# Optimization experiments

Measured on AMD Instinct MI355X. Metric: run time of the kernel, lower is better.

## Reference

```python
import jax, jax.numpy as jnp
import numpy as np

STRIDE = 16


def setup_inputs() -> dict:
    key = jax.random.key(0)
    kq, kk, kv, km = jax.random.split(key, 4)
    B, H, T, D = 2, 16, 2048, 64
    q = jax.random.normal(kq, (B, H, T, D), dtype=jnp.float32)
    k = jax.random.normal(kk, (B, H, T, D), dtype=jnp.float32)
    v = jax.random.normal(kv, (B, H, T, D), dtype=jnp.float32)
    mask = jax.random.randint(km, (B, 1, 1, T), 0, 2, dtype=jnp.int32)
    return {"q": q, "k": k, "v": v, "mask": mask}


def reference(q, k, v, mask):
    # q,k,v: (B,H,T,D); mask: (B,1,1,T_k)
    B, H, T_q, D = q.shape
    T_k = k.shape[2]
    scale = 1.0 / jnp.sqrt(jnp.float32(D))
    scores = jnp.einsum("bhqd,bhkd->bhqk", q, k) * scale
    rq = jnp.arange(T_q)[:, None]
    rk = jnp.arange(T_k)[None, :]
    stride_mask = (rk % STRIDE == 0) | (rq == rk)           # (T_q, T_k) bool
    NEG = jnp.float32(-1e9)
    scores = jnp.where(stride_mask[None, None], scores, NEG)
    scores = jnp.where(mask == 0, NEG, scores)
    attn = jax.nn.softmax(scores, axis=-1)
    out = jnp.einsum("bhqk,bhkd->bhqd", attn, v)
    return (out, attn)
```

## Files before the change

kernel.cpp:

```cpp
#include <hip/hip_runtime.h>
#include <hip/hip_bf16.h>

constexpr int B = 2, H = 16, T = 2048, D = 64;
constexpr int NS = T / 16;
constexpr int WAVES = 4, BLOCK = 256;
constexpr int CHUNKS = 32;
constexpr int ROWS_PER_BLOCK = T / CHUNKS;
constexpr int ROWS_PER_WAVE = ROWS_PER_BLOCK / WAVES;
constexpr int R = 4;
constexpr int GROUPS = ROWS_PER_WAVE / R;

__device__ __forceinline__ float rlf(float v, int l) {
    return __int_as_float(__builtin_amdgcn_readlane(__float_as_int(v), l));
}
__device__ __forceinline__ unsigned bf16rne(float f) {
    unsigned x = __float_as_uint(f);
    return (x + 0x7fffu + ((x >> 16) & 1u)) >> 16;
}
__device__ __forceinline__ float bflo(unsigned u) { return __uint_as_float(u << 16); }
__device__ __forceinline__ float bfhi(unsigned u) { return __uint_as_float(u & 0xffff0000u); }

__global__ __launch_bounds__(BLOCK, 4)
void strided_attn_kernel(const float* __restrict__ q,
                         const float* __restrict__ k,
                         const float* __restrict__ v,
                         const int*   __restrict__ mask,
                         float* __restrict__ out,
                         float* __restrict__ attn)
{
    __shared__ uint2    Ks2[NS][16];
    __shared__ unsigned Vp[NS / 2][64];
    __shared__ int      msk[NS];

    const int blk   = blockIdx.x;
    const int bh    = blk / CHUNKS;
    const int chunk = blk % CHUNKS;
    const int b     = bh / H;

    const float* qb = q + (size_t)bh * T * D;
    const float* kb = k + (size_t)bh * T * D;
    const float* vb = v + (size_t)bh * T * D;
    const int*   mb = mask + (size_t)b * T;

    const int tid = threadIdx.x;

    for (int i = tid; i < NS * 16; i += BLOCK) {
        const int j = i >> 4, c = i & 15;
        const float4 kv = *reinterpret_cast<const float4*>(kb + (size_t)(j * 16) * D + c * 4);
        uint2 pk;
        pk.x = bf16rne(kv.x) | (bf16rne(kv.y) << 16);
        pk.y = bf16rne(kv.z) | (bf16rne(kv.w) << 16);
        Ks2[j][c ^ (j & 15)] = pk;
    }
    for (int i = tid; i < (NS / 2) * 64; i += BLOCK) {
        const int j2 = i >> 6, d = i & 63;
        const float f0 = vb[(size_t)(32 * j2) * D + d];
        const float f1 = vb[(size_t)(32 * j2 + 16) * D + d];
        Vp[j2][d] = bf16rne(f0) | (bf16rne(f1) << 16);
    }
    if (tid < NS) msk[tid] = mb[tid * 16];

    const int wave = tid >> 6, lane = tid & 63;
    const int row0 = chunk * ROWS_PER_BLOCK + wave * ROWS_PER_WAVE;
    const int j0 = lane, j1 = lane + 64;
    const int xsw = lane & 15;
    const size_t bhT = (size_t)bh * T;

    const int mvals = (lane < ROWS_PER_WAVE) ? mb[row0 + lane] : 0;

    __syncthreads();

    const int m0 = msk[j0], m1 = msk[j1];

    #pragma unroll 1
    for (int g = 0; g < GROUPS; ++g) {
        const int grow = row0 + g * R;

        const float4 qv = *reinterpret_cast<const float4*>(qb + (size_t)grow * D + lane * 4);
        const float4 kg = *reinterpret_cast<const float4*>(kb + (size_t)grow * D + lane * 4);
        float vdr[R];
        #pragma unroll
        for (int r = 0; r < R; ++r)
            vdr[r] = vb[(size_t)(grow + r) * D + lane];

        float ds = fmaf(qv.w, kg.w, fmaf(qv.z, kg.z, fmaf(qv.y, kg.y, qv.x * kg.x)));
        ds += __shfl_xor(ds, 1, 64);
        ds += __shfl_xor(ds, 2, 64);
        ds += __shfl_xor(ds, 4, 64);
        ds += __shfl_xor(ds, 8, 64);
        const float sdv = ds * 0.125f;

        float s0[R] = {0.f, 0.f, 0.f, 0.f};
        float s1[R] = {0.f, 0.f, 0.f, 0.f};
        #pragma unroll 4
        for (int cq = 0; cq < 16; ++cq) {
            const uint2 a0 = Ks2[j0][cq ^ xsw];
            const uint2 a1 = Ks2[j1][cq ^ xsw];
            const float k0x = bflo(a0.x), k0y = bfhi(a0.x), k0z = bflo(a0.y), k0w = bfhi(a0.y);
            const float k1x = bflo(a1.x), k1y = bfhi(a1.x), k1z = bflo(a1.y), k1w = bfhi(a1.y);
            #pragma unroll
            for (int r = 0; r < R; ++r) {
                const int src = 16 * r + cq;
                const float qx = rlf(qv.x, src);
                const float qy = rlf(qv.y, src);
                const float qz = rlf(qv.z, src);
                const float qw = rlf(qv.w, src);
                s0[r] = fmaf(qw, k0w, fmaf(qz, k0z, fmaf(qy, k0y, fmaf(qx, k0x, s0[r]))));
                s1[r] = fmaf(qw, k1w, fmaf(qz, k1z, fmaf(qy, k1y, fmaf(qx, k1x, s1[r]))));
            }
        }

        float p0[R], p1[R], pd[R];
        #pragma unroll
        for (int r = 0; r < R; ++r) {
            float a0 = s0[r] * 0.125f, a1 = s1[r] * 0.125f;
            if (m0 == 0) a0 = -1e9f;
            if (m1 == 0) a1 = -1e9f;

            float sd = rlf(sdv, 16 * r);
            if (__builtin_amdgcn_readlane(mvals, g * R + r) == 0) sd = -1e9f;
            const bool qmod = (((g * R + r) & 15) == 0);

            const float e0 = __expf(a0);
            const float e1 = __expf(a1);
            const float ed = qmod ? 0.f : __expf(sd);
            float sum = e0 + e1;
            #pragma unroll
            for (int s = 32; s > 0; s >>= 1) sum += __shfl_xor(sum, s, 64);
            sum += ed;
            const float inv = 1.f / sum;

            p0[r] = e0 * inv;
            p1[r] = e1 * inv;
            pd[r] = ed * inv;
        }

        float acc[R];
        #pragma unroll
        for (int r = 0; r < R; ++r)
            acc[r] = pd[r] * vdr[r];

        #pragma unroll 8
        for (int j2 = 0; j2 < 32; ++j2) {
            const unsigned u = Vp[j2][lane];
            const float ve = bflo(u), vo = bfhi(u);
            #pragma unroll
            for (int r = 0; r < R; ++r)
                acc[r] = fmaf(rlf(p0[r], 2 * j2 + 1), vo,
                         fmaf(rlf(p0[r], 2 * j2), ve, acc[r]));
        }
        #pragma unroll 8
        for (int j2 = 32; j2 < 64; ++j2) {
            const unsigned u = Vp[j2][lane];
            const float ve = bflo(u), vo = bfhi(u);
            #pragma unroll
            for (int r = 0; r < R; ++r)
                acc[r] = fmaf(rlf(p1[r], 2 * (j2 - 32) + 1), vo,
                         fmaf(rlf(p1[r], 2 * (j2 - 32)), ve, acc[r]));
        }

        #pragma unroll
        for (int r = 0; r < R; ++r)
            out[(bhT + grow + r) * D + lane] = acc[r];

        #pragma unroll 1
        for (int t = 0; t < 8; ++t) {
            const int f    = t * 64 + lane;
            const int idx2 = ((t & 3) * 16) + (lane >> 2);
            #pragma unroll
            for (int r = 0; r < R; ++r) {
                const int qrow = grow + r;
                const float psrc = (t < 4) ? p0[r] : p1[r];
                const float pg   = __shfl(psrc, idx2, 64);
                float4 val = make_float4(0.f, 0.f, 0.f, 0.f);
                if ((lane & 3) == 0) val.x = pg;
                const bool qmod = (((g * R + r) & 15) == 0);
                const int  fq   = qrow >> 2;
                if (!qmod && t == (fq >> 6) && lane == (fq & 63)) {
                    if      (r == 0) val.x = pd[r];
                    else if (r == 1) val.y = pd[r];
                    else if (r == 2) val.z = pd[r];
                    else             val.w = pd[r];
                }
                *reinterpret_cast<float4*>(attn + (bhT + qrow) * (size_t)T + 4 * f) = val;
            }
        }
    }
}

extern "C" void kernel_launch(void* const* d_in, const int* in_sizes, int n_in,
                              void* d_out, int out_size, void* d_ws, size_t ws_size,
                              hipStream_t stream) {
    const float* q    = (const float*)d_in[0];
    const float* k    = (const float*)d_in[1];
    const float* v    = (const float*)d_in[2];
    const int*   mask = (const int*)d_in[3];

    float* out  = (float*)d_out;
    float* attn = out + (size_t)B * H * T * D;

    dim3 grid(B * H * CHUNKS);
    dim3 block(BLOCK);
    hipLaunchKernelGGL(strided_attn_kernel, grid, block, 0, stream,
                       q, k, v, mask, out, attn);
}
```

Baseline: 145.3 us.

## Process eight query rows per group, preload Q, and reswizzle K LDS layout

Doubles the rows handled per group from four to eight, so each K read from LDS and each V read are reused across twice as many query rows. All four Q row-vectors the wave needs are loaded once before the loop instead of reloading Q per group. The K shared-memory swizzle gains an extra XOR term meant to cut bank conflicts. The cost is more registers for the accumulators and probabilities, which may hurt occupancy under the launch-bounds limit.

```diff
diff --git a/kernel.cpp b/kernel.cpp
--- a/kernel.cpp
+++ b/kernel.cpp
@@ -7,7 +7,7 @@
 constexpr int CHUNKS = 32;
 constexpr int ROWS_PER_BLOCK = T / CHUNKS;
 constexpr int ROWS_PER_WAVE = ROWS_PER_BLOCK / WAVES;
-constexpr int R = 4;
+constexpr int R = 8;
 constexpr int GROUPS = ROWS_PER_WAVE / R;
 
 __device__ __forceinline__ float rlf(float v, int l) {
@@ -19,6 +19,10 @@
 }
 __device__ __forceinline__ float bflo(unsigned u) { return __uint_as_float(u << 16); }
 __device__ __forceinline__ float bfhi(unsigned u) { return __uint_as_float(u & 0xffff0000u); }
+
+__device__ __forceinline__ int kslot(int c, int j) {
+    return c ^ (j & 15) ^ (((j >> 4) & 3) << 2);
+}
 
 __global__ __launch_bounds__(BLOCK, 4)
 void strided_attn_kernel(const float* __restrict__ q,
@@ -50,7 +54,7 @@
         uint2 pk;
         pk.x = bf16rne(kv.x) | (bf16rne(kv.y) << 16);
         pk.y = bf16rne(kv.z) | (bf16rne(kv.w) << 16);
-        Ks2[j][c ^ (j & 15)] = pk;
+        Ks2[j][kslot(c, j)] = pk;
     }
     for (int i = tid; i < (NS / 2) * 64; i += BLOCK) {
         const int j2 = i >> 6, d = i & 63;
@@ -63,10 +67,15 @@
     const int wave = tid >> 6, lane = tid & 63;
     const int row0 = chunk * ROWS_PER_BLOCK + wave * ROWS_PER_WAVE;
     const int j0 = lane, j1 = lane + 64;
-    const int xsw = lane & 15;
+    const int xsw = (lane & 15) ^ (((lane >> 4) & 3) << 2);
     const size_t bhT = (size_t)bh * T;
 
     const int mvals = (lane < ROWS_PER_WAVE) ? mb[row0 + lane] : 0;
+
+    const float4 qv0  = *reinterpret_cast<const float4*>(qb + (size_t)(row0     ) * D + lane * 4);
+    const float4 qv20 = *reinterpret_cast<const float4*>(qb + (size_t)(row0 +  4) * D + lane * 4);
+    const float4 qv1  = *reinterpret_cast<const float4*>(qb + (size_t)(row0 +  8) * D + lane * 4);
+    const float4 qv21 = *reinterpret_cast<const float4*>(qb + (size_t)(row0 + 12) * D + lane * 4);
 
     __syncthreads();
 
@@ -76,22 +85,19 @@
     for (int g = 0; g < GROUPS; ++g) {
         const int grow = row0 + g * R;
 
-        const float4 qv = *reinterpret_cast<const float4*>(qb + (size_t)grow * D + lane * 4);
-        const float4 kg = *reinterpret_cast<const float4*>(kb + (size_t)grow * D + lane * 4);
+        const float4 kg  = *reinterpret_cast<const float4*>(kb + (size_t)(grow    ) * D + lane * 4);
+        const float4 kg2 = *reinterpret_cast<const float4*>(kb + (size_t)(grow + 4) * D + lane * 4);
         float vdr[R];
         #pragma unroll
         for (int r = 0; r < R; ++r)
             vdr[r] = vb[(size_t)(grow + r) * D + lane];
 
-        float ds = fmaf(qv.w, kg.w, fmaf(qv.z, kg.z, fmaf(qv.y, kg.y, qv.x * kg.x)));
-        ds += __shfl_xor(ds, 1, 64);
-        ds += __shfl_xor(ds, 2, 64);
-        ds += __shfl_xor(ds, 4, 64);
-        ds += __shfl_xor(ds, 8, 64);
-        const float sdv = ds * 0.125f;
-
-        float s0[R] = {0.f, 0.f, 0.f, 0.f};
-        float s1[R] = {0.f, 0.f, 0.f, 0.f};
+        const float4 qsel  = (g == 0) ? qv0  : qv1;
+        const float4 qsel2 = (g == 0) ? qv20 : qv21;
+
+        float s0[R], s1[R];
+        #pragma unroll
+        for (int r = 0; r < R; ++r) { s0[r] = 0.f; s1[r] = 0.f; }
         #pragma unroll 4
         for (int cq = 0; cq < 16; ++cq) {
             const uint2 a0 = Ks2[j0][cq ^ xsw];
@@ -100,15 +106,28 @@
             const float k1x = bflo(a1.x), k1y = bfhi(a1.x), k1z = bflo(a1.y), k1w = bfhi(a1.y);
             #pragma unroll
             for (int r = 0; r < R; ++r) {
-                const int src = 16 * r + cq;
-                const float qx = rlf(qv.x, src);
-                const float qy = rlf(qv.y, src);
-                const float qz = rlf(qv.z, src);
-                const float qw = rlf(qv.w, src);
+                const int src = 16 * (r & 3) + cq;
+                const float qx = rlf((r < 4) ? qsel.x : qsel2.x, src);
+                const float qy = rlf((r < 4) ? qsel.y : qsel2.y, src);
+                const float qz = rlf((r < 4) ? qsel.z : qsel2.z, src);
+                const float qw = rlf((r < 4) ? qsel.w : qsel2.w, src);
                 s0[r] = fmaf(qw, k0w, fmaf(qz, k0z, fmaf(qy, k0y, fmaf(qx, k0x, s0[r]))));
                 s1[r] = fmaf(qw, k1w, fmaf(qz, k1z, fmaf(qy, k1y, fmaf(qx, k1x, s1[r]))));
             }
         }
+
+        float ds = fmaf(qsel.w, kg.w, fmaf(qsel.z, kg.z, fmaf(qsel.y, kg.y, qsel.x * kg.x)));
+        ds += __shfl_xor(ds, 1, 64);
+        ds += __shfl_xor(ds, 2, 64);
+        ds += __shfl_xor(ds, 4, 64);
+        ds += __shfl_xor(ds, 8, 64);
+        const float sdv = ds * 0.125f;
+        float ds2 = fmaf(qsel2.w, kg2.w, fmaf(qsel2.z, kg2.z, fmaf(qsel2.y, kg2.y, qsel2.x * kg2.x)));
+        ds2 += __shfl_xor(ds2, 1, 64);
+        ds2 += __shfl_xor(ds2, 2, 64);
+        ds2 += __shfl_xor(ds2, 4, 64);
+        ds2 += __shfl_xor(ds2, 8, 64);
+        const float sdv2 = ds2 * 0.125f;
 
         float p0[R], p1[R], pd[R];
         #pragma unroll
@@ -117,7 +136,7 @@
             if (m0 == 0) a0 = -1e9f;
             if (m1 == 0) a1 = -1e9f;
 
-            float sd = rlf(sdv, 16 * r);
+            float sd = (r < 4) ? rlf(sdv, 16 * r) : rlf(sdv2, 16 * (r - 4));
             if (__builtin_amdgcn_readlane(mvals, g * R + r) == 0) sd = -1e9f;
             const bool qmod = (((g * R + r) & 15) == 0);
 
@@ -177,10 +196,11 @@
                 const bool qmod = (((g * R + r) & 15) == 0);
                 const int  fq   = qrow >> 2;
                 if (!qmod && t == (fq >> 6) && lane == (fq & 63)) {
-                    if      (r == 0) val.x = pd[r];
-                    else if (r == 1) val.y = pd[r];
-                    else if (r == 2) val.z = pd[r];
-                    else             val.w = pd[r];
+                    const int dc = r & 3;
+                    if      (dc == 0) val.x = pd[r];
+                    else if (dc == 1) val.y = pd[r];
+                    else if (dc == 2) val.z = pd[r];
+                    else              val.w = pd[r];
                 }
                 *reinterpret_cast<float4*>(attn + (bhT + qrow) * (size_t)T + 4 * f) = val;
             }
```

Result: faster. 137.2 us (-5.5%).
